# Kernel optimization log

Hardware: AMD Instinct MI355X
Metric: run time of the kernel (lower is better)

The kernel has to match this reference:

```python
import jax, jax.numpy as jnp
import numpy as np

B, H, S, D = 4, 16, 2048, 64
NEG = -1e9


def setup_inputs() -> dict:
    key = jax.random.key(0)
    kq, kk, kv, km = jax.random.split(key, 4)
    query = jax.random.normal(kq, (B, H, S, D), dtype=jnp.float32)
    k_ = jax.random.normal(kk, (B, H, S, D), dtype=jnp.float32)
    v_ = jax.random.normal(kv, (B, H, S, D), dtype=jnp.float32)
    mask = jax.random.randint(km, (B, S, S), 0, 2, dtype=jnp.int32)
    return {"query": query, "key": k_, "value": v_, "mask": mask}


def reference(query, key, value, mask):
    # scores: [B, H, S, S]
    scale = 1.0 / jnp.sqrt(jnp.asarray(query.shape[-1], query.dtype))
    scores = jnp.einsum('bhqd,bhkd->bhqk', query, key) * scale
    # mask [B,S,S] -> [B,1,S,S], broadcast over heads; masked_fill(mask==0, -1e9)
    scores = jnp.where(mask[:, None, :, :] == 0, jnp.asarray(NEG, scores.dtype), scores)
    attn = jax.nn.softmax(scores, axis=-1)
    return jnp.einsum('bhqk,bhkd->bhqd', attn, value)
```

## Files before the change

kernel.cpp:

```cpp
#include <hip/hip_runtime.h>
#include <stdint.h>


#define SQ 2048
#define DD 64

typedef __attribute__((ext_vector_type(8))) short short8;
typedef __attribute__((ext_vector_type(4))) short bshort4;
typedef __attribute__((ext_vector_type(4))) float f32x4;

union U8 { uint32_t u[4]; short8 s; };
union U4 { uint32_t u[2]; bshort4 s; };

__device__ __forceinline__ uint32_t pk_rne(float lo, float hi) {
  uint32_t a = __builtin_bit_cast(uint32_t, lo) + 0x8000u;
  uint32_t b = __builtin_bit_cast(uint32_t, hi) + 0x8000u;
  return __builtin_amdgcn_perm(b, a, 0x07060302u);
}
__device__ __forceinline__ uint32_t pk_tr(float lo, float hi) {
  return __builtin_amdgcn_perm(__builtin_bit_cast(uint32_t, hi),
                               __builtin_bit_cast(uint32_t, lo), 0x07060302u);
}

#if __has_builtin(__builtin_amdgcn_exp2f)
#define EXP2(x) __builtin_amdgcn_exp2f(x)
#else
#define EXP2(x) __exp2f(x)
#endif

__device__ __forceinline__ f32x4 mfma32(short8 a, short8 b, f32x4 c) {
  return __builtin_amdgcn_mfma_f32_16x16x32_bf16(a, b, c, 0, 0, 0);
}

#if __has_builtin(__builtin_amdgcn_mfma_f32_16x16x16bf16_1k)
__device__ __forceinline__ f32x4 mfma16(bshort4 a, bshort4 b, f32x4 c) {
  return __builtin_amdgcn_mfma_f32_16x16x16bf16_1k(a, b, c, 0, 0, 0);
}
#else
__device__ __forceinline__ f32x4 mfma16(bshort4 a, bshort4 b, f32x4 c) {
  asm("v_mfma_f32_16x16x16_bf16 %0, %1, %2, %0" : "+v"(c) : "v"(a), "v"(b));
  return c;
}
#endif

__global__ __launch_bounds__(256) void pack_mask_kernel(const int* __restrict__ m,
                                                        uint32_t* __restrict__ bits) {
  int i = blockIdx.x * 256 + threadIdx.x;
  const int4* p = (const int4*)m + (size_t)i * 8;
  uint32_t wrd = 0;
#pragma unroll
  for (int j = 0; j < 8; ++j) {
    int4 v = p[j];
    wrd |= (v.x != 0 ? 1u : 0u) << (4 * j + 0);
    wrd |= (v.y != 0 ? 1u : 0u) << (4 * j + 1);
    wrd |= (v.z != 0 ? 1u : 0u) << (4 * j + 2);
    wrd |= (v.w != 0 ? 1u : 0u) << (4 * j + 3);
  }
  bits[i] = wrd;
}

template <bool USE_BITS>
__global__ __launch_bounds__(256, 2) void attn_kernel(
    const float* __restrict__ Qg, const float* __restrict__ Kg,
    const float* __restrict__ Vg, const int* __restrict__ Mg,
    const uint32_t* __restrict__ bits, float* __restrict__ Og) {
  __shared__ __align__(16) short sK[2][64 * 72];
  __shared__ __align__(16) short sVT[2][64 * 72];

  const int tid = threadIdx.x;
  const int lane = tid & 63;
  const int wv = tid >> 6;
  const int l15 = lane & 15;
  const int quad = lane >> 4;

  const int bid = blockIdx.x;
  const int h = bid & 15;
  const int qt = (bid >> 4) & 7;
  const int b = bid >> 7;

  const size_t bh = (size_t)b * 16 + h;
  const float* Qp = Qg + bh * (size_t)(SQ * DD);
  const float* Kp = Kg + bh * (size_t)(SQ * DD);
  const float* Vp = Vg + bh * (size_t)(SQ * DD);
  float* Op = Og + bh * (size_t)(SQ * DD);
  const int q0w = qt * 256 + wv * 64;
  const int brow = b * SQ;

  const float QS = 0.18033688f;
  const float NC = -17.312340f;
  const float NINF = -__builtin_inff();

  short8 qf[4][2];
#pragma unroll
  for (int g = 0; g < 4; ++g)
#pragma unroll
    for (int dc = 0; dc < 2; ++dc) {
      const float* src = Qp + (size_t)(q0w + g * 16 + l15) * DD + dc * 32 + quad * 8;
      float4 a = *(const float4*)src;
      float4 c = *(const float4*)(src + 4);
      U8 t;
      t.u[0] = pk_rne(a.x * QS, a.y * QS);
      t.u[1] = pk_rne(a.z * QS, a.w * QS);
      t.u[2] = pk_rne(c.x * QS, c.y * QS);
      t.u[3] = pk_rne(c.z * QS, c.w * QS);
      qf[g][dc] = t.s;
    }

  f32x4 o[4][4];
#pragma unroll
  for (int g = 0; g < 4; ++g)
#pragma unroll
    for (int dc = 0; dc < 4; ++dc) o[g][dc] = (f32x4){0.f, 0.f, 0.f, 0.f};
  float lacc[4] = {0.f, 0.f, 0.f, 0.f};

  const int kr = lane;
  const int kcb = wv * 16;
  const int vr2 = (lane & 31) * 2;
  const int vcb = wv * 16 + (lane >> 5) * 8;
  const float* kbase = Kp + (size_t)kr * DD + kcb;
  const float* vbase = Vp + (size_t)vr2 * DD + vcb;

  float4 kA, kB, kC, kD, vA, vB, vC, vD;
  uint2 mwc[4], mwn[4];

  {
    const float4* kp = (const float4*)kbase;
    kA = kp[0]; kB = kp[1]; kC = kp[2]; kD = kp[3];
    const float* r0 = vbase;
    vA = ((const float4*)r0)[0]; vB = ((const float4*)r0)[1];
    vC = ((const float4*)(r0 + DD))[0]; vD = ((const float4*)(r0 + DD))[1];
    if (USE_BITS) {
#pragma unroll
      for (int g = 0; g < 4; ++g)
        mwc[g] = *(const uint2*)&bits[(size_t)(brow + q0w + g * 16 + l15) * (SQ / 32)];
    }
    U8 w0, w1;
    w0.u[0] = pk_rne(kA.x, kA.y); w0.u[1] = pk_rne(kA.z, kA.w);
    w0.u[2] = pk_rne(kB.x, kB.y); w0.u[3] = pk_rne(kB.z, kB.w);
    w1.u[0] = pk_rne(kC.x, kC.y); w1.u[1] = pk_rne(kC.z, kC.w);
    w1.u[2] = pk_rne(kD.x, kD.y); w1.u[3] = pk_rne(kD.z, kD.w);
    *(short8*)&sK[0][kr * 72 + kcb] = w0.s;
    *(short8*)&sK[0][kr * 72 + kcb + 8] = w1.s;
    float av[8] = {vA.x, vA.y, vA.z, vA.w, vB.x, vB.y, vB.z, vB.w};
    float bv[8] = {vC.x, vC.y, vC.z, vC.w, vD.x, vD.y, vD.z, vD.w};
#pragma unroll
    for (int j = 0; j < 8; ++j)
      *(uint32_t*)&sVT[0][(vcb + j) * 72 + vr2] = pk_rne(av[j], bv[j]);
  }

  for (int kt = 0; kt < SQ / 64; ++kt) {
    const int buf = kt & 1;
    const int k0 = kt * 64;

    __syncthreads();

    if (kt + 1 < SQ / 64) {
      const float4* kp = (const float4*)(kbase + (size_t)(k0 + 64) * DD);
      kA = kp[0]; kB = kp[1]; kC = kp[2]; kD = kp[3];
      const float* r0 = vbase + (size_t)(k0 + 64) * DD;
      vA = ((const float4*)r0)[0]; vB = ((const float4*)r0)[1];
      vC = ((const float4*)(r0 + DD))[0]; vD = ((const float4*)(r0 + DD))[1];
      if (USE_BITS) {
#pragma unroll
        for (int g = 0; g < 4; ++g)
          mwn[g] = *(const uint2*)&bits[(size_t)(brow + q0w + g * 16 + l15) * (SQ / 32) + (kt + 1) * 2];
      }
    }

    const short* sKb = sK[buf];
    const short* sVb = sVT[buf];
#pragma unroll
    for (int kb = 0; kb < 4; ++kb) {
      short8 kfa = *(const short8*)&sKb[(kb * 16 + l15) * 72 + quad * 8];
      short8 kfb = *(const short8*)&sKb[(kb * 16 + l15) * 72 + 32 + quad * 8];
      bshort4 vf[4];
#pragma unroll
      for (int dc = 0; dc < 4; ++dc)
        vf[dc] = *(const bshort4*)&sVb[(dc * 16 + l15) * 72 + kb * 16 + quad * 4];

#pragma unroll
      for (int g = 0; g < 4; ++g) {
        uint32_t t;
        if (USE_BITS) {
          uint32_t w = (kb & 2) ? mwc[g].y : mwc[g].x;
          t = w >> ((kb & 1) * 16 + quad * 4);
        } else {
          const int* mrow = Mg + (size_t)(brow + q0w + g * 16 + l15) * SQ + k0 + kb * 16 + quad * 4;
          t = (mrow[0] != 0) | ((mrow[1] != 0) << 1) | ((mrow[2] != 0) << 2) |
              ((mrow[3] != 0) << 3);
        }
        f32x4 ci;
        ci[0] = (t & 1) ? NC : NINF;
        ci[1] = (t & 2) ? NC : NINF;
        ci[2] = (t & 4) ? NC : NINF;
        ci[3] = (t & 8) ? NC : NINF;
        f32x4 st = mfma32(kfa, qf[g][0], ci);
        st = mfma32(kfb, qf[g][1], st);
        float p0 = EXP2(st[0]);
        float p1 = EXP2(st[1]);
        float p2 = EXP2(st[2]);
        float p3 = EXP2(st[3]);
        lacc[g] += (p0 + p1) + (p2 + p3);
        U4 pw;
        pw.u[0] = pk_tr(p0, p1);
        pw.u[1] = pk_tr(p2, p3);
#pragma unroll
        for (int dc = 0; dc < 4; ++dc)
          o[g][dc] = mfma16(pw.s, vf[dc], o[g][dc]);
      }
    }

    if (kt + 1 < SQ / 64) {
      short* dK = (short*)sK[buf ^ 1];
      short* dV = (short*)sVT[buf ^ 1];
      U8 w0, w1;
      w0.u[0] = pk_rne(kA.x, kA.y); w0.u[1] = pk_rne(kA.z, kA.w);
      w0.u[2] = pk_rne(kB.x, kB.y); w0.u[3] = pk_rne(kB.z, kB.w);
      w1.u[0] = pk_rne(kC.x, kC.y); w1.u[1] = pk_rne(kC.z, kC.w);
      w1.u[2] = pk_rne(kD.x, kD.y); w1.u[3] = pk_rne(kD.z, kD.w);
      *(short8*)&dK[kr * 72 + kcb] = w0.s;
      *(short8*)&dK[kr * 72 + kcb + 8] = w1.s;
      float av[8] = {vA.x, vA.y, vA.z, vA.w, vB.x, vB.y, vB.z, vB.w};
      float bv[8] = {vC.x, vC.y, vC.z, vC.w, vD.x, vD.y, vD.z, vD.w};
#pragma unroll
      for (int j = 0; j < 8; ++j)
        *(uint32_t*)&dV[(vcb + j) * 72 + vr2] = pk_rne(av[j], bv[j]);
      if (USE_BITS) {
#pragma unroll
        for (int g = 0; g < 4; ++g) mwc[g] = mwn[g];
      }
    }
  }

#pragma unroll
  for (int g = 0; g < 4; ++g) {
    float ls = lacc[g];
    ls += __shfl_xor(ls, 16);
    ls += __shfl_xor(ls, 32);
    float inv = 1.0f / ls;
#pragma unroll
    for (int r = 0; r < 4; ++r) {
      float invr = __shfl(inv, quad * 4 + r);
      float* dst = Op + (size_t)(q0w + g * 16 + quad * 4 + r) * DD + l15;
      dst[0]  = o[g][0][r] * invr;
      dst[16] = o[g][1][r] * invr;
      dst[32] = o[g][2][r] * invr;
      dst[48] = o[g][3][r] * invr;
    }
  }
}

extern "C" void kernel_launch(void* const* d_in, const int* in_sizes, int n_in,
                              void* d_out, int out_size, void* d_ws, size_t ws_size,
                              hipStream_t stream) {
  const float* Q = (const float*)d_in[0];
  const float* K = (const float*)d_in[1];
  const float* V = (const float*)d_in[2];
  const int* M = (const int*)d_in[3];
  float* out = (float*)d_out;

  const size_t bits_bytes = (size_t)4 * SQ * SQ / 8;
  const int attn_blocks = 4 * (SQ / 256) * 16;

  if (ws_size >= bits_bytes) {
    uint32_t* bits = (uint32_t*)d_ws;
    const int words = 4 * SQ * (SQ / 32);
    pack_mask_kernel<<<words / 256, 256, 0, stream>>>(M, bits);
    attn_kernel<true><<<attn_blocks, 256, 0, stream>>>(Q, K, V, M, bits, out);
  } else {
    attn_kernel<false><<<attn_blocks, 256, 0, stream>>>(Q, K, V, M, nullptr, out);
  }
}
```

Before: 307.0 us.

## Halve per-block query tile, compute row sums via MFMA, ballot-based mask packing

Each block now handles 128 query rows (32 per wave) instead of 256, doubling the grid to 1024 blocks and raising launch bounds to 4 blocks per CU. This trades more K/V reloads per head for higher occupancy. The softmax denominator is now taken from an extra MFMA against a ones vector rather than scalar adds and cross-lane shuffles. The mask packer switches to a grid-stride loop using wave ballot with coalesced int loads.

```diff
diff --git a/kernel.cpp b/kernel.cpp
--- a/kernel.cpp
+++ b/kernel.cpp
@@ -45,22 +45,19 @@
 
 __global__ __launch_bounds__(256) void pack_mask_kernel(const int* __restrict__ m,
                                                         uint32_t* __restrict__ bits) {
-  int i = blockIdx.x * 256 + threadIdx.x;
-  const int4* p = (const int4*)m + (size_t)i * 8;
-  uint32_t wrd = 0;
-#pragma unroll
-  for (int j = 0; j < 8; ++j) {
-    int4 v = p[j];
-    wrd |= (v.x != 0 ? 1u : 0u) << (4 * j + 0);
-    wrd |= (v.y != 0 ? 1u : 0u) << (4 * j + 1);
-    wrd |= (v.z != 0 ? 1u : 0u) << (4 * j + 2);
-    wrd |= (v.w != 0 ? 1u : 0u) << (4 * j + 3);
-  }
-  bits[i] = wrd;
+  const int lane = threadIdx.x & 63;
+  const int wid = (blockIdx.x * 256 + threadIdx.x) >> 6;
+  const int nw = (gridDim.x * 256) >> 6;
+  const size_t total = (size_t)4 * SQ * SQ;
+  for (size_t base = (size_t)wid * 64; base < total; base += (size_t)nw * 64) {
+    int v = m[base + lane];
+    unsigned long long b = __ballot(v != 0);
+    if (lane == 0) *(unsigned long long*)&bits[base >> 5] = b;
+  }
 }
 
 template <bool USE_BITS>
-__global__ __launch_bounds__(256, 2) void attn_kernel(
+__global__ __launch_bounds__(256, 4) void attn_kernel(
     const float* __restrict__ Qg, const float* __restrict__ Kg,
     const float* __restrict__ Vg, const int* __restrict__ Mg,
     const uint32_t* __restrict__ bits, float* __restrict__ Og) {
@@ -75,24 +72,27 @@
 
   const int bid = blockIdx.x;
   const int h = bid & 15;
-  const int qt = (bid >> 4) & 7;
-  const int b = bid >> 7;
+  const int qt = (bid >> 4) & 15;
+  const int b = bid >> 8;
 
   const size_t bh = (size_t)b * 16 + h;
   const float* Qp = Qg + bh * (size_t)(SQ * DD);
   const float* Kp = Kg + bh * (size_t)(SQ * DD);
   const float* Vp = Vg + bh * (size_t)(SQ * DD);
   float* Op = Og + bh * (size_t)(SQ * DD);
-  const int q0w = qt * 256 + wv * 64;
+  const int q0w = qt * 128 + wv * 32;
   const int brow = b * SQ;
 
   const float QS = 0.18033688f;
   const float NC = -17.312340f;
   const float NINF = -__builtin_inff();
 
-  short8 qf[4][2];
-#pragma unroll
-  for (int g = 0; g < 4; ++g)
+  U4 onesu; onesu.u[0] = 0x3f803f80u; onesu.u[1] = 0x3f803f80u;
+  const bshort4 ones = onesu.s;
+
+  short8 qf[2][2];
+#pragma unroll
+  for (int g = 0; g < 2; ++g)
 #pragma unroll
     for (int dc = 0; dc < 2; ++dc) {
       const float* src = Qp + (size_t)(q0w + g * 16 + l15) * DD + dc * 32 + quad * 8;
@@ -106,12 +106,14 @@
       qf[g][dc] = t.s;
     }
 
-  f32x4 o[4][4];
-#pragma unroll
-  for (int g = 0; g < 4; ++g)
+  f32x4 o[2][4];
+  f32x4 osum[2];
+#pragma unroll
+  for (int g = 0; g < 2; ++g) {
 #pragma unroll
     for (int dc = 0; dc < 4; ++dc) o[g][dc] = (f32x4){0.f, 0.f, 0.f, 0.f};
-  float lacc[4] = {0.f, 0.f, 0.f, 0.f};
+    osum[g] = (f32x4){0.f, 0.f, 0.f, 0.f};
+  }
 
   const int kr = lane;
   const int kcb = wv * 16;
@@ -121,7 +123,7 @@
   const float* vbase = Vp + (size_t)vr2 * DD + vcb;
 
   float4 kA, kB, kC, kD, vA, vB, vC, vD;
-  uint2 mwc[4], mwn[4];
+  uint2 mwc[2], mwn[2];
 
   {
     const float4* kp = (const float4*)kbase;
@@ -131,7 +133,7 @@
     vC = ((const float4*)(r0 + DD))[0]; vD = ((const float4*)(r0 + DD))[1];
     if (USE_BITS) {
 #pragma unroll
-      for (int g = 0; g < 4; ++g)
+      for (int g = 0; g < 2; ++g)
         mwc[g] = *(const uint2*)&bits[(size_t)(brow + q0w + g * 16 + l15) * (SQ / 32)];
     }
     U8 w0, w1;
@@ -162,7 +164,7 @@
       vC = ((const float4*)(r0 + DD))[0]; vD = ((const float4*)(r0 + DD))[1];
       if (USE_BITS) {
 #pragma unroll
-        for (int g = 0; g < 4; ++g)
+        for (int g = 0; g < 2; ++g)
           mwn[g] = *(const uint2*)&bits[(size_t)(brow + q0w + g * 16 + l15) * (SQ / 32) + (kt + 1) * 2];
       }
     }
@@ -179,7 +181,7 @@
         vf[dc] = *(const bshort4*)&sVb[(dc * 16 + l15) * 72 + kb * 16 + quad * 4];
 
 #pragma unroll
-      for (int g = 0; g < 4; ++g) {
+      for (int g = 0; g < 2; ++g) {
         uint32_t t;
         if (USE_BITS) {
           uint32_t w = (kb & 2) ? mwc[g].y : mwc[g].x;
@@ -200,13 +202,13 @@
         float p1 = EXP2(st[1]);
         float p2 = EXP2(st[2]);
         float p3 = EXP2(st[3]);
-        lacc[g] += (p0 + p1) + (p2 + p3);
         U4 pw;
         pw.u[0] = pk_tr(p0, p1);
         pw.u[1] = pk_tr(p2, p3);
 #pragma unroll
         for (int dc = 0; dc < 4; ++dc)
           o[g][dc] = mfma16(pw.s, vf[dc], o[g][dc]);
+        osum[g] = mfma16(pw.s, ones, osum[g]);
       }
     }
 
@@ -227,25 +229,21 @@
         *(uint32_t*)&dV[(vcb + j) * 72 + vr2] = pk_rne(av[j], bv[j]);
       if (USE_BITS) {
 #pragma unroll
-        for (int g = 0; g < 4; ++g) mwc[g] = mwn[g];
+        for (int g = 0; g < 2; ++g) mwc[g] = mwn[g];
       }
     }
   }
 
 #pragma unroll
-  for (int g = 0; g < 4; ++g) {
-    float ls = lacc[g];
-    ls += __shfl_xor(ls, 16);
-    ls += __shfl_xor(ls, 32);
-    float inv = 1.0f / ls;
+  for (int g = 0; g < 2; ++g) {
 #pragma unroll
     for (int r = 0; r < 4; ++r) {
-      float invr = __shfl(inv, quad * 4 + r);
+      float inv = 1.0f / osum[g][r];
       float* dst = Op + (size_t)(q0w + g * 16 + quad * 4 + r) * DD + l15;
-      dst[0]  = o[g][0][r] * invr;
-      dst[16] = o[g][1][r] * invr;
-      dst[32] = o[g][2][r] * invr;
-      dst[48] = o[g][3][r] * invr;
+      dst[0]  = o[g][0][r] * inv;
+      dst[16] = o[g][1][r] * inv;
+      dst[32] = o[g][2][r] * inv;
+      dst[48] = o[g][3][r] * inv;
     }
   }
 }
@@ -260,12 +258,11 @@
   float* out = (float*)d_out;
 
   const size_t bits_bytes = (size_t)4 * SQ * SQ / 8;
-  const int attn_blocks = 4 * (SQ / 256) * 16;
+  const int attn_blocks = 4 * (SQ / 128) * 16;
 
   if (ws_size >= bits_bytes) {
     uint32_t* bits = (uint32_t*)d_ws;
-    const int words = 4 * SQ * (SQ / 32);
-    pack_mask_kernel<<<words / 256, 256, 0, stream>>>(M, bits);
+    pack_mask_kernel<<<2048, 256, 0, stream>>>(M, bits);
     attn_kernel<true><<<attn_blocks, 256, 0, stream>>>(Q, K, V, M, bits, out);
   } else {
     attn_kernel<false><<<attn_blocks, 256, 0, stream>>>(Q, K, V, M, nullptr, out);
```

New measurement: 346.1 us. +12.7%, slower.
